# Kernel tuning notes

Hardware: AMD Instinct MI355X
Metric: run time of the kernel (lower is better)

The kernel has to match this reference:

```python
import math
import jax, jax.numpy as jnp
import numpy as np

EPS = 1e-8


def setup_inputs() -> dict:
    key = jax.random.key(0)
    k0, k1, k2, k3 = jax.random.split(key, 4)
    B, C_IN, C_OUT, H, W, K, S = 8, 256, 256, 128, 128, 3, 512
    return {
        "input": jax.random.normal(k0, (B, C_IN, H, W), dtype=jnp.float32),
        "style": jax.random.normal(k1, (B, S), dtype=jnp.float32),
        # learned params
        "weight": jax.random.normal(k2, (1, C_OUT, C_IN, K, K), dtype=jnp.float32),
        "mod_weight": jax.random.normal(k3, (C_IN, S), dtype=jnp.float32),
        "mod_bias": jnp.ones((C_IN,), dtype=jnp.float32),  # bias_init=1
    }


def reference(input, style, weight, mod_weight, mod_bias):
    B, C_in, H, W = input.shape
    _, C_out, _, K, _ = weight.shape
    S = mod_weight.shape[1]

    # EqualLinear modulation: F.linear(style, w * (1/sqrt(S))) + bias (lr_mul=1)
    lin_scale = 1.0 / math.sqrt(S)
    s = style @ (mod_weight.T * lin_scale) + mod_bias  # [B, C_in]

    # per-sample weight modulation
    conv_scale = 1.0 / math.sqrt(C_in * K * K)  # fan_in scale
    w = conv_scale * weight * s[:, None, :, None, None]  # [B, C_out, C_in, K, K]

    # demodulation
    demod = jax.lax.rsqrt(jnp.sum(w * w, axis=(2, 3, 4)) + EPS)  # [B, C_out]
    w = w * demod[:, :, None, None, None]

    # groups=batch conv2d with padding=k//2 (same spatial size)
    pad = K // 2

    def conv_one(x, wk):  # x: [C_in, H, W], wk: [C_out, C_in, K, K]
        y = jax.lax.conv_general_dilated(
            x[None], wk, window_strides=(1, 1),
            padding=[(pad, pad), (pad, pad)],
            dimension_numbers=("NCHW", "OIHW", "NCHW"))
        return y[0]

    return jax.vmap(conv_one)(input, w)  # [B, C_out, H, W]
```

## Files before the change

### kernel.cpp

```cpp
#include <hip/hip_runtime.h>
#include <hip/hip_bf16.h>

typedef __attribute__((ext_vector_type(8))) short short8;
typedef __attribute__((ext_vector_type(4))) float floatx4;
typedef __attribute__((ext_vector_type(4))) unsigned uint4v;

#define B_ 8
#define C_IN 256
#define C_OUT 256
#define H_ 128
#define W_ 128
#define S_ 512
#define HW_ (H_*W_)
#define LIN_SCALE 0.04419417382415922f
#define CONV_SCALE 0.02083333333333333f
#define EPS_ 1e-8f

#define XPH 130
#define XPW 136
#define TTH 8
#define TTW 32
#define PH2 10
#define PW2 34
#define NPIX2 (PH2*PW2)
#define BUFSZ 24576
#define ABUFSZ 8192
#define ABASE_LDS 49152
#define NKB 72
#define NTHR 256

__device__ __forceinline__ unsigned short f2bf(float f) {
  unsigned u = __builtin_bit_cast(unsigned, f);
  u = (u + 0x7fffu + ((u >> 16) & 1u)) >> 16;
  return (unsigned short)u;
}
__device__ __forceinline__ unsigned pack2(float a, float b) {
  return (unsigned)f2bf(a) | ((unsigned)f2bf(b) << 16);
}
__device__ __forceinline__ void gload16(const void* g, void* l) {
  __builtin_amdgcn_global_load_lds(
      (const __attribute__((address_space(1))) unsigned*)g,
      (__attribute__((address_space(3))) unsigned*)l, 16, 0, 0);
}

__global__ void k_style(const float* __restrict__ style, const float* __restrict__ mw,
                        const float* __restrict__ mb, float* __restrict__ s) {
  __shared__ float sty[S_];
  const int b = blockIdx.x;
  for (int i = threadIdx.x; i < S_; i += 256) sty[i] = style[b*S_ + i];
  __syncthreads();
  const int ci = threadIdx.x;
  const float* wr = mw + (size_t)ci*S_;
  float acc = 0.f;
  for (int i = 0; i < S_; ++i) acc += sty[i] * wr[i];
  s[b*C_IN + ci] = acc * LIN_SCALE + mb[ci];
}

__global__ void k_demod(const float* __restrict__ weight, const float* __restrict__ s,
                        float* __restrict__ demod) {
  const int b = blockIdx.x >> 8, co = blockIdx.x & 255;
  const int l = threadIdx.x;
  const float* wrow = weight + (size_t)co*C_IN*9;
  const float* sb = s + b*C_IN;
  float acc = 0.f;
  for (int idx = l; idx < C_IN*9; idx += 64) {
    float wv = wrow[idx] * sb[idx/9];
    acc += wv*wv;
  }
#pragma unroll
  for (int off = 32; off; off >>= 1) acc += __shfl_down(acc, off, 64);
  if (l == 0) demod[blockIdx.x] = rsqrtf(acc * (CONV_SCALE*CONV_SCALE) + EPS_);
}

__global__ void k_pack(const float* __restrict__ weight, const float* __restrict__ s,
                       const float* __restrict__ demod, unsigned short* __restrict__ frag) {
  const int bid = blockIdx.x;
  const int mt = bid & 15;
  const int chunk = (bid >> 4) & 7;
  const int b  = bid >> 7;
  const int l = threadIdx.x;
  const int co = mt*16 + (l & 15);
  const float dm = demod[b*C_OUT + co] * CONV_SCALE;
  const float* sb = s + b*C_IN;
  unsigned v[9][4];
#pragma unroll
  for (int jj = 0; jj < 4; ++jj) {
    int ci0 = chunk*32 + (l >> 4)*8 + jj*2;
    float w0[9], w1[9];
    __builtin_memcpy(w0, weight + ((size_t)co*C_IN + ci0    )*9, 36);
    __builtin_memcpy(w1, weight + ((size_t)co*C_IN + ci0 + 1)*9, 36);
    float s0 = sb[ci0] * dm, s1 = sb[ci0 + 1] * dm;
#pragma unroll
    for (int r = 0; r < 9; ++r)
      v[r][jj] = pack2(w0[r]*s0, w1[r]*s1);
  }
#pragma unroll
  for (int r = 0; r < 9; ++r) {
    unsigned* dst = (unsigned*)(frag +
        ((size_t)((b*NKB + chunk*9 + r)*16 + mt))*512 + l*8);
    dst[0] = v[r][0]; dst[1] = v[r][1]; dst[2] = v[r][2]; dst[3] = v[r][3];
  }
}

__global__ void k_xpose(const float* __restrict__ x, unsigned short* __restrict__ xp) {
  __shared__ __align__(16) unsigned lds32[64*128];
  const int bid = blockIdx.x;
  const int half = bid & 1, h = (bid >> 1) & 127, b = bid >> 8;
  const int w0 = half*64;
  const int t = threadIdx.x;
  const uint4v z = {0u,0u,0u,0u};
  if (t < 32) {
    int chunk = t >> 2, part = t & 3;
    unsigned short* p = xp +
        (((size_t)(b*8 + chunk)*XPH + (h + 1))*XPW + half*129)*32 + part*8;
    *(uint4v*)p = z;
  }
  if (h == 0) {
    for (int i = t; i < 65*2*8*4; i += 256) {
      int part = i & 3, cell = i >> 2;
      int wwi = cell % 65; int rest = cell / 65;
      int rowsel = rest & 1, chunk = rest >> 1;
      unsigned short* p = xp +
          (((size_t)(b*8 + chunk)*XPH + rowsel*129)*XPW + (half*65 + wwi))*32 + part*8;
      *(uint4v*)p = z;
    }
  }
  const float* xr = x + (size_t)b*C_IN*HW_ + (size_t)h*W_ + w0;
#pragma unroll
  for (int j = 0; j < 8; ++j) {
    int cp = j*16 + (t >> 4);
    int ci = cp*2;
    const float* p0 = xr + (size_t)ci*HW_ + (t & 15)*4;
    floatx4 f0 = *(const floatx4*)p0;
    floatx4 f1 = *(const floatx4*)(p0 + HW_);
    int g = cp >> 2, slot = cp & 3;
#pragma unroll
    for (int k = 0; k < 4; ++k) {
      int px = (t & 15)*4 + k;
      lds32[px*128 + ((g ^ ((px >> 2) & 7)) << 2) + slot] = pack2(f0[k], f1[k]);
    }
  }
  __syncthreads();
#pragma unroll
  for (int i = 0; i < 8; ++i) {
    int item = i*256 + t;
    int px = item >> 5, g = item & 31;
    int c = (item >> 2) & 7, sub = item & 3;
    int gs = g ^ ((px >> 2) & 7);
    uint4v v = *(const uint4v*)&lds32[px*128 + (gs << 2)];
    unsigned short* dst = xp +
        (((size_t)(b*8 + c)*XPH + (h + 1))*XPW + (w0 + 1 + px))*32 + sub*8;
    *(uint4v*)dst = v;
  }
}

__launch_bounds__(NTHR, 2)
__global__ void k_conv(const unsigned short* __restrict__ xpad,
                       const unsigned short* __restrict__ frag,
                       float* __restrict__ out) {
  __shared__ __align__(16) unsigned char sm[2*BUFSZ + 4*ABUFSZ];
  const int work = (blockIdx.x & 7)*128 + (blockIdx.x >> 3);
  const int ct = work & 1;
  const int w2 = work >> 1;
  const int sx = w2 & 3, sy = (w2 >> 2) & 15, b = w2 >> 6;
  const int h0 = sy*TTH, w0 = sx*TTW;
  const int tid = threadIdx.x;
  const int lane = tid & 63, wv = tid >> 6;
  const int wm = wv >> 1, wn = wv & 1;
  const int sl = lane >> 4, c15 = lane & 15, wn8 = wn*8;
  const int b8 = b*8;

  floatx4 acc[4][8];
#pragma unroll
  for (int m = 0; m < 4; ++m)
#pragma unroll
    for (int n = 0; n < 8; ++n) acc[m][n] = floatx4{0.f, 0.f, 0.f, 0.f};

  int srcoff[6];
#pragma unroll
  for (int p = 0; p < 6; ++p) {
    int item = p*256 + tid;
    int px = item >> 2, q8s = item & 3;
    if (px > NPIX2 - 1) px = NPIX2 - 1;
    int ph = px / PW2, pw = px - ph*PW2;
    int q8 = q8s ^ ((px >> 1) & 3);
    srcoff[p] = (ph*XPW + pw)*32 + q8*8;
  }
  const unsigned short* abase = frag + ((size_t)b*NKB*16 + ct*8)*512 + (size_t)tid*8;
  const unsigned char* aRd = sm + ABASE_LDS + wm*4096 + lane*16;

  short8 Ar[4], Br[8];

  auto readRegs = [&](int slot, int bbase, int tap) __attribute__((always_inline)) {
    const int dh = tap/3, dw = tap%3;
#pragma unroll
    for (int m = 0; m < 4; ++m)
      Ar[m] = *(const short8*)(aRd + slot*8192 + m*1024);
#pragma unroll
    for (int n = 0; n < 8; ++n) {
      int nt = wn8 + n;
      int pix = ((nt >> 1) + dh)*PW2 + ((nt & 1)*16 + c15 + dw);
      int addr = pix*64 + ((sl ^ ((pix >> 1) & 3)) << 4);
      Br[n] = *(const short8*)(sm + bbase + addr);
    }
  };
  auto mfmaStep = [&]() __attribute__((always_inline)) {
    __builtin_amdgcn_s_setprio(1);
#pragma unroll
    for (int n = 0; n < 8; ++n) {
      acc[0][n] = __builtin_amdgcn_mfma_f32_16x16x32_bf16(Ar[0], Br[n], acc[0][n], 0, 0, 0);
      acc[1][n] = __builtin_amdgcn_mfma_f32_16x16x32_bf16(Ar[1], Br[n], acc[1][n], 0, 0, 0);
      acc[2][n] = __builtin_amdgcn_mfma_f32_16x16x32_bf16(Ar[2], Br[n], acc[2][n], 0, 0, 0);
      acc[3][n] = __builtin_amdgcn_mfma_f32_16x16x32_bf16(Ar[3], Br[n], acc[3][n], 0, 0, 0);
    }
    __builtin_amdgcn_s_setprio(0);
  };

#define SBAR0 __builtin_amdgcn_sched_barrier(0)
#define WAITB(NLIT) do { SBAR0; \
    asm volatile("s_waitcnt vmcnt(" NLIT ")" ::: "memory"); \
    __builtin_amdgcn_s_barrier(); SBAR0; } while (0)

#define STEP(J, R, NLIT) do { \
    WAITB(NLIT); \
    { int kbs = c9 + (R) + 3; if (kbs > NKB-1) kbs = NKB-1; \
      const unsigned short* asrc = abase + (size_t)kbs*8192; \
      unsigned char* adst = sm + ABASE_LDS + ((((J)+(R)+3)&3)*8192) + tid*16; \
      gload16(asrc, adst); gload16(asrc + 2048, adst + 4096); } \
    if ((R) < 6) \
      gload16(xc + srcoff[R], sm + ((((J)+1)&1)*BUFSZ) + ((R)*256 + tid)*16); \
    mfmaStep(); \
    readRegs(((J)+(R)+1)&3, \
             ((R)==8) ? ((((J)+1)&1)*BUFSZ) : (((J)&1)*BUFSZ), \
             ((R)==8) ? 0 : (R)+1); \
  } while (0)

#define CHUNK(J) do { \
    const int c = cc*4 + (J); const int c9 = c*9; \
    const int cn = (c < 7) ? c + 1 : 7; \
    const unsigned short* xc = xpad + (((size_t)(b8 + cn)*XPH + h0)*XPW + w0)*32; \
    STEP(J,0,"2"); STEP(J,1,"3"); STEP(J,2,"4"); \
    STEP(J,3,"4"); STEP(J,4,"4"); STEP(J,5,"4"); \
    STEP(J,6,"4"); STEP(J,7,"3"); STEP(J,8,"2"); \
  } while (0)

  {
    const unsigned short* xc0 = xpad + (((size_t)b8*XPH + h0)*XPW + w0)*32;
#pragma unroll
    for (int p = 0; p < 6; ++p)
      gload16(xc0 + srcoff[p], sm + (p*256 + tid)*16);
#pragma unroll
    for (int s5 = 0; s5 < 3; ++s5) {
      const unsigned short* asrc = abase + (size_t)s5*8192;
      unsigned char* adst = sm + ABASE_LDS + s5*8192 + tid*16;
      gload16(asrc, adst); gload16(asrc + 2048, adst + 4096);
    }
    SBAR0;
    asm volatile("s_waitcnt vmcnt(0)" ::: "memory");
    __builtin_amdgcn_s_barrier();
    SBAR0;
    readRegs(0, 0, 0);
  }

#pragma unroll 1
  for (int cc = 0; cc < 2; ++cc) {
    CHUNK(0); CHUNK(1); CHUNK(2); CHUNK(3);
  }
#undef CHUNK
#undef STEP
#undef WAITB
#undef SBAR0

  float* ob = out + ((size_t)b*C_OUT + ct*128)*HW_;
  const int tw = lane & 15, rg = lane >> 4;
#pragma unroll
  for (int m = 0; m < 4; ++m) {
#pragma unroll
    for (int n = 0; n < 8; ++n) {
      int co = (wm*4 + m)*16 + rg*4;
      int nt = wn8 + n;
      int h = h0 + (nt >> 1);
      int w = w0 + (nt & 1)*16 + tw;
      float* p = ob + (size_t)co*HW_ + (size_t)h*W_ + w;
#pragma unroll
      for (int i = 0; i < 4; ++i) p[i*HW_] = acc[m][n][i];
    }
  }
}

extern "C" void kernel_launch(void* const* d_in, const int* in_sizes, int n_in,
                              void* d_out, int out_size, void* d_ws, size_t ws_size,
                              hipStream_t stream) {
  const float* x      = (const float*)d_in[0];
  const float* style  = (const float*)d_in[1];
  const float* weight = (const float*)d_in[2];
  const float* mod_w  = (const float*)d_in[3];
  const float* mod_b  = (const float*)d_in[4];
  float* out = (float*)d_out;
  char* ws = (char*)d_ws;

  float* s     = (float*)ws;
  float* demod = (float*)(ws + 8192);
  unsigned short* frag = (unsigned short*)(ws + 16384);
  unsigned short* xpad = (unsigned short*)(ws + (16u<<20));

  k_style<<<B_, 256, 0, stream>>>(style, mod_w, mod_b, s);
  k_demod<<<B_*C_OUT, 64, 0, stream>>>(weight, s, demod);
  k_pack<<<B_*8*16, 64, 0, stream>>>(weight, s, demod, frag);
  k_xpose<<<B_*H_*2, 256, 0, stream>>>(x, xpad);
  k_conv<<<B_*2*16*4, NTHR, 0, stream>>>(xpad, frag, out);
}
```

Before: 201.0 us.

## Load weight fragments directly into registers and cut per-tap barriers

Weight (A) fragments are no longer staged through LDS with async global-to-LDS loads. Each wave now loads its own fragments straight from global memory into double-buffered registers (pa/pb), one tap ahead. Block barriers drop from one per tap to one mid-chunk barrier plus one at chunk end, and LDS use falls to the input tiles only, which could allow higher occupancy. The trade-offs are global-load latency exposed to the MFMA loop with only one step of prefetch, more VGPR pressure, and redundant global reads of the same fragments across waves.

```diff
diff --git a/kernel.cpp b/kernel.cpp
--- a/kernel.cpp
+++ b/kernel.cpp
@@ -24,8 +24,6 @@
 #define PW2 34
 #define NPIX2 (PH2*PW2)
 #define BUFSZ 24576
-#define ABUFSZ 8192
-#define ABASE_LDS 49152
 #define NKB 72
 #define NTHR 256
 
@@ -158,7 +156,7 @@
 __global__ void k_conv(const unsigned short* __restrict__ xpad,
                        const unsigned short* __restrict__ frag,
                        float* __restrict__ out) {
-  __shared__ __align__(16) unsigned char sm[2*BUFSZ + 4*ABUFSZ];
+  __shared__ __align__(16) unsigned char sm[2*BUFSZ];
   const int work = (blockIdx.x & 7)*128 + (blockIdx.x >> 3);
   const int ct = work & 1;
   const int w2 = work >> 1;
@@ -186,16 +184,20 @@
     int q8 = q8s ^ ((px >> 1) & 3);
     srcoff[p] = (ph*XPW + pw)*32 + q8*8;
   }
-  const unsigned short* abase = frag + ((size_t)b*NKB*16 + ct*8)*512 + (size_t)tid*8;
-  const unsigned char* aRd = sm + ABASE_LDS + wm*4096 + lane*16;
-
-  short8 Ar[4], Br[8];
-
-  auto readRegs = [&](int slot, int bbase, int tap) __attribute__((always_inline)) {
+  const unsigned short* abase = frag +
+      ((size_t)b*NKB*16 + ct*8 + wm*4)*512 + (size_t)lane*8;
+
+  short8 pa[4], pb[4], Br[8];
+
+  auto loadA = [&](short8* dst, int kb) __attribute__((always_inline)) {
+    const unsigned short* src = abase + (size_t)kb*8192;
+    dst[0] = *(const short8*)(src);
+    dst[1] = *(const short8*)(src + 512);
+    dst[2] = *(const short8*)(src + 1024);
+    dst[3] = *(const short8*)(src + 1536);
+  };
+  auto readBr = [&](int bbase, int tap) __attribute__((always_inline)) {
     const int dh = tap/3, dw = tap%3;
-#pragma unroll
-    for (int m = 0; m < 4; ++m)
-      Ar[m] = *(const short8*)(aRd + slot*8192 + m*1024);
 #pragma unroll
     for (int n = 0; n < 8; ++n) {
       int nt = wn8 + n;
@@ -204,44 +206,42 @@
       Br[n] = *(const short8*)(sm + bbase + addr);
     }
   };
-  auto mfmaStep = [&]() __attribute__((always_inline)) {
+  auto mfmaStep = [&](const short8* A) __attribute__((always_inline)) {
     __builtin_amdgcn_s_setprio(1);
 #pragma unroll
     for (int n = 0; n < 8; ++n) {
-      acc[0][n] = __builtin_amdgcn_mfma_f32_16x16x32_bf16(Ar[0], Br[n], acc[0][n], 0, 0, 0);
-      acc[1][n] = __builtin_amdgcn_mfma_f32_16x16x32_bf16(Ar[1], Br[n], acc[1][n], 0, 0, 0);
-      acc[2][n] = __builtin_amdgcn_mfma_f32_16x16x32_bf16(Ar[2], Br[n], acc[2][n], 0, 0, 0);
-      acc[3][n] = __builtin_amdgcn_mfma_f32_16x16x32_bf16(Ar[3], Br[n], acc[3][n], 0, 0, 0);
+      acc[0][n] = __builtin_amdgcn_mfma_f32_16x16x32_bf16(A[0], Br[n], acc[0][n], 0, 0, 0);
+      acc[1][n] = __builtin_amdgcn_mfma_f32_16x16x32_bf16(A[1], Br[n], acc[1][n], 0, 0, 0);
+      acc[2][n] = __builtin_amdgcn_mfma_f32_16x16x32_bf16(A[2], Br[n], acc[2][n], 0, 0, 0);
+      acc[3][n] = __builtin_amdgcn_mfma_f32_16x16x32_bf16(A[3], Br[n], acc[3][n], 0, 0, 0);
     }
     __builtin_amdgcn_s_setprio(0);
   };
 
 #define SBAR0 __builtin_amdgcn_sched_barrier(0)
-#define WAITB(NLIT) do { SBAR0; \
-    asm volatile("s_waitcnt vmcnt(" NLIT ")" ::: "memory"); \
+#define MIDBAR do { SBAR0; \
+    asm volatile("s_waitcnt vmcnt(4)" ::: "memory"); \
     __builtin_amdgcn_s_barrier(); SBAR0; } while (0)
 
-#define STEP(J, R, NLIT) do { \
-    WAITB(NLIT); \
-    { int kbs = c9 + (R) + 3; if (kbs > NKB-1) kbs = NKB-1; \
-      const unsigned short* asrc = abase + (size_t)kbs*8192; \
-      unsigned char* adst = sm + ABASE_LDS + ((((J)+(R)+3)&3)*8192) + tid*16; \
-      gload16(asrc, adst); gload16(asrc + 2048, adst + 4096); } \
-    if ((R) < 6) \
+#define STEP(J, R) do { \
+    SBAR0; \
+    { int kbs = c9 + (R) + 1; if (kbs > NKB-1) kbs = NKB-1; \
+      loadA((((J)+(R)) & 1) ? pa : pb, kbs); } \
+    if ((R) < 6 && c < 7) \
       gload16(xc + srcoff[R], sm + ((((J)+1)&1)*BUFSZ) + ((R)*256 + tid)*16); \
-    mfmaStep(); \
-    readRegs(((J)+(R)+1)&3, \
-             ((R)==8) ? ((((J)+1)&1)*BUFSZ) : (((J)&1)*BUFSZ), \
-             ((R)==8) ? 0 : (R)+1); \
+    mfmaStep((((J)+(R)) & 1) ? pb : pa); \
+    readBr((((R)==8) ? (((J)+1)&1) : ((J)&1))*BUFSZ, ((R)==8) ? 0 : (R)+1); \
   } while (0)
 
 #define CHUNK(J) do { \
     const int c = cc*4 + (J); const int c9 = c*9; \
     const int cn = (c < 7) ? c + 1 : 7; \
     const unsigned short* xc = xpad + (((size_t)(b8 + cn)*XPH + h0)*XPW + w0)*32; \
-    STEP(J,0,"2"); STEP(J,1,"3"); STEP(J,2,"4"); \
-    STEP(J,3,"4"); STEP(J,4,"4"); STEP(J,5,"4"); \
-    STEP(J,6,"4"); STEP(J,7,"3"); STEP(J,8,"2"); \
+    STEP(J,0); STEP(J,1); STEP(J,2); STEP(J,3); \
+    STEP(J,4); STEP(J,5); STEP(J,6); STEP(J,7); \
+    MIDBAR; \
+    STEP(J,8); \
+    if (c < 7) { SBAR0; __builtin_amdgcn_s_barrier(); SBAR0; } \
   } while (0)
 
   {
@@ -249,17 +249,12 @@
 #pragma unroll
     for (int p = 0; p < 6; ++p)
       gload16(xc0 + srcoff[p], sm + (p*256 + tid)*16);
-#pragma unroll
-    for (int s5 = 0; s5 < 3; ++s5) {
-      const unsigned short* asrc = abase + (size_t)s5*8192;
-      unsigned char* adst = sm + ABASE_LDS + s5*8192 + tid*16;
-      gload16(asrc, adst); gload16(asrc + 2048, adst + 4096);
-    }
+    loadA(pa, 0);
     SBAR0;
     asm volatile("s_waitcnt vmcnt(0)" ::: "memory");
     __builtin_amdgcn_s_barrier();
     SBAR0;
-    readRegs(0, 0, 0);
+    readBr(0, 0);
   }
 
 #pragma unroll 1
@@ -268,7 +263,7 @@
   }
 #undef CHUNK
 #undef STEP
-#undef WAITB
+#undef MIDBAR
 #undef SBAR0
 
   float* ob = out + ((size_t)b*C_OUT + ct*128)*HW_;
```

Result: slower. 212.6 us (+5.8%).
